# Optimization experiments

Measured on AMD Instinct MI355X. Metric: run time of the kernel, lower is better.

Reference implementation:

```python
import jax, jax.numpy as jnp
import numpy as np

PAD = 0
N_SENSE = 3
VOCAB = 100000
OUT_VOCAB = 50000
D = 128
B = 64
MAX_LEN = 512


def setup_inputs() -> dict:
    key = jax.random.key(0)
    ks = jax.random.split(key, 8)
    inputs = jax.random.randint(ks[0], (B, MAX_LEN * N_SENSE), 0, VOCAB, dtype=jnp.int64 if jax.config.jax_enable_x64 else jnp.int32)
    length_weights = jax.random.uniform(ks[1], (B, 1, 1), dtype=jnp.float32, minval=0.1, maxval=1.0)
    word_attn_mask = jax.random.bernoulli(ks[2], 0.1, (B, MAX_LEN))
    embedding = jax.random.normal(ks[3], (VOCAB, D), dtype=jnp.float32) * 0.02
    W_attn = jax.random.normal(ks[4], (1, D), dtype=jnp.float32) * 0.02
    b_attn = jnp.zeros((1,), dtype=jnp.float32)
    W_lin = jax.random.normal(ks[5], (OUT_VOCAB, D), dtype=jnp.float32) * 0.02
    b_lin = jnp.zeros((OUT_VOCAB,), dtype=jnp.float32)
    return {"inputs": inputs, "length_weights": length_weights, "word_attn_mask": word_attn_mask,
            "embedding": embedding, "W_attn": W_attn, "b_attn": b_attn, "W_lin": W_lin, "b_lin": b_lin}


def reference(inputs, length_weights, word_attn_mask, embedding, W_attn, b_attn, W_lin, b_lin):
    Bsz, LS = inputs.shape
    L = LS // N_SENSE
    # padding row contributes zeros (nn.Embedding padding_idx=PAD)
    E = embedding.at[PAD].set(0.0)
    embeds = E[inputs]                                   # [B, L*S, D]
    embeds4 = embeds.reshape(Bsz, L, N_SENSE, -1)
    embed_mean = embeds4.mean(axis=2)                    # [B, L, D]
    # word-level attention: Linear(D,1) -> mask -> softmax over words
    word_imp = jnp.einsum('bld,d->bl', embed_mean, W_attn[0]) + b_attn[0]
    word_imp = jnp.where(word_attn_mask, -jnp.inf, word_imp)
    word_w = jax.nn.softmax(word_imp, axis=-1)           # [B, L]
    context = jnp.einsum('bl,bld->bd', word_w, embed_mean)  # [B, D]
    # sense-level attention: similarity of each sense embedding to context
    sim = jnp.einsum('bnd,bd->bn', embeds, context)      # [B, L*S]
    sense_w = jax.nn.softmax(sim.reshape(Bsz, L, N_SENSE), axis=-1).reshape(Bsz, LS)
    attn_w = length_weights.reshape(Bsz, 1) * sense_w    # scale by 1/length
    attn_w = jnp.where(inputs == PAD, 0.0, attn_w)
    hidden = jnp.einsum('bn,bnd->bd', attn_w, embeds)    # [B, D]
    logits = hidden @ W_lin.T + b_lin                    # [B, OUT_VOCAB]
    return jax.nn.log_softmax(logits, axis=-1)
```

## Files before the change

### kernel.cpp

```cpp
#include <hip/hip_runtime.h>
#include <math.h>

#define B_    64
#define L_    512
#define S_    3
#define D_    128
#define OV_   50000
#define VOC_  100000
#define NBLK_ 782

typedef __attribute__((ext_vector_type(8))) short bf16x8;
typedef __attribute__((ext_vector_type(4))) float f32x4;

__device__ __forceinline__ float waveReduceSum(float v) {
#pragma unroll
    for (int off = 32; off >= 1; off >>= 1) v += __shfl_xor(v, off, 64);
    return v;
}
__device__ __forceinline__ float waveReduceMax(float v) {
#pragma unroll
    for (int off = 32; off >= 1; off >>= 1) v = fmaxf(v, __shfl_xor(v, off, 64));
    return v;
}

__device__ __forceinline__ short f2bf(float f) {
    unsigned int u = __float_as_uint(f);
    return (short)((u + 0x7FFFu + ((u >> 16) & 1u)) >> 16);
}

__global__ __launch_bounds__(256) void prequery_kernel(
    const float* __restrict__ emb, const float* __restrict__ Wa,
    float* __restrict__ P, float* __restrict__ context,
    float* __restrict__ hidden)
{
    const int tid = threadIdx.x;
    if (blockIdx.x < 64 && tid < D_) {
        context[blockIdx.x * D_ + tid] = 0.f;
        hidden[blockIdx.x * D_ + tid]  = 0.f;
    }

    const int lane = tid & 63;
    const int q = lane >> 4;
    const int j = lane & 15;
    const int waveg = blockIdx.x * 4 + (tid >> 6);
    const int nwaves = gridDim.x * 4;

    const float4 wa0 = ((const float4*)Wa)[2 * j];
    const float4 wa1 = ((const float4*)Wa)[2 * j + 1];

    for (int r0 = waveg * 4; r0 < VOC_; r0 += nwaves * 4) {
        const float4* row = (const float4*)(emb + (long)(r0 + q) * D_ + j * 8);
        float4 e0 = row[0], e1 = row[1];
        float s = e0.x * wa0.x + e0.y * wa0.y + e0.z * wa0.z + e0.w * wa0.w
                + e1.x * wa1.x + e1.y * wa1.y + e1.z * wa1.z + e1.w * wa1.w;
#pragma unroll
        for (int off = 8; off >= 1; off >>= 1) s += __shfl_xor(s, off, 64);
        if (j == 0) P[r0 + q] = s;
    }
}

__device__ __forceinline__ void word_softmax(
    const int* in_b, const int* __restrict__ mask, const float* __restrict__ P,
    float babias, int b, float* s_imp, float* s_red)
{
    const int tid = threadIdx.x;
    const int wave = tid >> 6, lane = tid & 63;

    int   idx[2][S_];
    float pv[2][S_];
#pragma unroll
    for (int half = 0; half < 2; ++half) {
        const int l = tid + half * 256;
#pragma unroll
        for (int s = 0; s < S_; ++s) {
            idx[half][s] = in_b[l * S_ + s];
            pv[half][s]  = P[idx[half][s]];
        }
    }
#pragma unroll
    for (int half = 0; half < 2; ++half) {
        const int l = tid + half * 256;
        float acc = 0.f;
#pragma unroll
        for (int s = 0; s < S_; ++s)
            acc += (idx[half][s] != 0) ? pv[half][s] : 0.f;
        float imp = acc * (1.0f / 3.0f) + babias;
        s_imp[l] = mask[b * L_ + l] ? -INFINITY : imp;
    }
    __syncthreads();

    float v0 = s_imp[tid], v1 = s_imp[tid + 256];
    float m = waveReduceMax(fmaxf(v0, v1));
    if (lane == 0) s_red[wave] = m;
    __syncthreads();
    m = fmaxf(fmaxf(s_red[0], s_red[1]), fmaxf(s_red[2], s_red[3]));
    __syncthreads();
    float p0 = expf(v0 - m), p1 = expf(v1 - m);
    float ssum = waveReduceSum(p0 + p1);
    if (lane == 0) s_red[wave] = ssum;
    __syncthreads();
    float inv = (1.0f / 3.0f) / (s_red[0] + s_red[1] + s_red[2] + s_red[3]);
    s_imp[tid]       = p0 * inv;
    s_imp[tid + 256] = p1 * inv;
    __syncthreads();
}

__global__ __launch_bounds__(256) void context_kernel(
    const int* __restrict__ inputs, const int* __restrict__ mask,
    const float* __restrict__ P, const float* __restrict__ ba,
    const float* __restrict__ emb, float* __restrict__ context)
{
    const int b    = blockIdx.x >> 4;
    const int base = (blockIdx.x & 15) * 32;
    const int tid  = threadIdx.x;
    const int wave = tid >> 6, lane = tid & 63;
    const int h = lane >> 5, j = lane & 31;

    __shared__ float s_imp[L_];
    __shared__ float s_red[4];
    __shared__ float s_part[8][D_];
    __shared__ int   s_idx[32 * S_];

    const int* in_b = inputs + b * (L_ * S_);
    if (tid < 32 * S_) s_idx[tid] = in_b[base * S_ + tid];
    word_softmax(in_b, mask, P, ba[0], b, s_imp, s_red);

    int    idx[4][S_];
    float4 e[4][S_];
#pragma unroll
    for (int it = 0; it < 4; ++it) {
        const int lw = (wave + it * 4) * 2 + h;
#pragma unroll
        for (int s = 0; s < S_; ++s) {
            idx[it][s] = s_idx[lw * S_ + s];
            e[it][s]   = ((const float4*)(emb + (long)idx[it][s] * D_))[j];
        }
    }

    float4 c = make_float4(0.f, 0.f, 0.f, 0.f);
#pragma unroll
    for (int it = 0; it < 4; ++it) {
        const int lw = (wave + it * 4) * 2 + h;
        const float w = s_imp[base + lw];
#pragma unroll
        for (int s = 0; s < S_; ++s) {
            const float ws = (idx[it][s] != 0) ? w : 0.f;
            c.x += ws * e[it][s].x; c.y += ws * e[it][s].y;
            c.z += ws * e[it][s].z; c.w += ws * e[it][s].w;
        }
    }
    ((float4*)s_part[wave * 2 + h])[j] = c;
    __syncthreads();
    if (tid < D_) {
        float acc = 0.f;
#pragma unroll
        for (int p = 0; p < 8; ++p) acc += s_part[p][tid];
        atomicAdd(&context[b * D_ + tid], acc);
    }
}

__global__ __launch_bounds__(256) void sense_kernel(
    const int* __restrict__ inputs, const float* __restrict__ lwp,
    const float* __restrict__ context, const float* __restrict__ emb,
    float* __restrict__ hidden)
{
    const int b    = blockIdx.x >> 5;
    const int base = (blockIdx.x & 31) * 16;
    const int tid  = threadIdx.x;
    const int wave = tid >> 6, lane = tid & 63;
    const int h = lane >> 5, j = lane & 31;

    __shared__ float s_part[8][D_];
    __shared__ int   s_idx[16 * S_];

    const int* in_b = inputs + b * (L_ * S_);
    if (tid < 16 * S_) s_idx[tid] = in_b[base * S_ + tid];
    __syncthreads();

    const float lwb = lwp[b];
    const float4 c4 = ((const float4*)(context + b * D_))[j];

    int    idx[2][S_];
    float4 e[2][S_];
#pragma unroll
    for (int it = 0; it < 2; ++it) {
        const int lw = (wave + it * 4) * 2 + h;
#pragma unroll
        for (int s = 0; s < S_; ++s) {
            idx[it][s] = s_idx[lw * S_ + s];
            e[it][s]   = ((const float4*)(emb + (long)idx[it][s] * D_))[j];
        }
    }

    float4 hacc = make_float4(0.f, 0.f, 0.f, 0.f);
#pragma unroll
    for (int it = 0; it < 2; ++it) {
        float sim[S_];
#pragma unroll
        for (int s = 0; s < S_; ++s)
            sim[s] = e[it][s].x * c4.x + e[it][s].y * c4.y
                   + e[it][s].z * c4.z + e[it][s].w * c4.w;
#pragma unroll
        for (int off = 16; off >= 1; off >>= 1) {
            sim[0] += __shfl_xor(sim[0], off, 64);
            sim[1] += __shfl_xor(sim[1], off, 64);
            sim[2] += __shfl_xor(sim[2], off, 64);
        }
        sim[0] = (idx[it][0] != 0) ? sim[0] : 0.f;
        sim[1] = (idx[it][1] != 0) ? sim[1] : 0.f;
        sim[2] = (idx[it][2] != 0) ? sim[2] : 0.f;
        float e0 = expf(sim[0]), e1 = expf(sim[1]), e2 = expf(sim[2]);
        float f = lwb / (e0 + e1 + e2);
        float w0 = (idx[it][0] != 0) ? e0 * f : 0.f;
        float w1 = (idx[it][1] != 0) ? e1 * f : 0.f;
        float w2 = (idx[it][2] != 0) ? e2 * f : 0.f;
        hacc.x += w0 * e[it][0].x + w1 * e[it][1].x + w2 * e[it][2].x;
        hacc.y += w0 * e[it][0].y + w1 * e[it][1].y + w2 * e[it][2].y;
        hacc.z += w0 * e[it][0].z + w1 * e[it][1].z + w2 * e[it][2].z;
        hacc.w += w0 * e[it][0].w + w1 * e[it][1].w + w2 * e[it][2].w;
    }
    ((float4*)s_part[wave * 2 + h])[j] = hacc;
    __syncthreads();
    if (tid < D_) {
        float acc = 0.f;
#pragma unroll
        for (int p = 0; p < 8; ++p) acc += s_part[p][tid];
        atomicAdd(&hidden[b * D_ + tid], acc);
    }
}

__global__ __launch_bounds__(256) void logits_kernel(
    const float* __restrict__ hidden, const float* __restrict__ Wl,
    const float* __restrict__ bl, float* __restrict__ logits,
    float* __restrict__ pS)
{
    __shared__ short s_hbf[64][136];
    const int tid  = threadIdx.x;
    const int wave = tid >> 6, lane = tid & 63;
    const int m15  = lane & 15, quad = lane >> 4;
    const int v    = blockIdx.x * 64 + wave * 16 + m15;
    const bool valid = (v < OV_);
    const int vc   = valid ? v : (OV_ - 1);

    for (int i = tid; i < 2048; i += 256) {
        float4 x = ((const float4*)hidden)[i];
        const int r = i >> 5;
        const int c = (i & 31) * 4;
        short* dst = &s_hbf[r][c];
        dst[0] = f2bf(x.x); dst[1] = f2bf(x.y);
        dst[2] = f2bf(x.z); dst[3] = f2bf(x.w);
    }
    __syncthreads();

    f32x4 acc[4];
#pragma unroll
    for (int t = 0; t < 4; ++t) acc[t] = (f32x4){0.f, 0.f, 0.f, 0.f};

    const float* wrow = Wl + (long)vc * D_ + quad * 8;
#pragma unroll
    for (int ks = 0; ks < 4; ++ks) {
        float4 x0 = *(const float4*)(wrow + ks * 32);
        float4 x1 = *(const float4*)(wrow + ks * 32 + 4);
        bf16x8 bfr;
        bfr[0] = f2bf(x0.x); bfr[1] = f2bf(x0.y); bfr[2] = f2bf(x0.z); bfr[3] = f2bf(x0.w);
        bfr[4] = f2bf(x1.x); bfr[5] = f2bf(x1.y); bfr[6] = f2bf(x1.z); bfr[7] = f2bf(x1.w);
#pragma unroll
        for (int t = 0; t < 4; ++t) {
            bf16x8 afr = *(const bf16x8*)&s_hbf[t * 16 + m15][ks * 32 + quad * 8];
            acc[t] = __builtin_amdgcn_mfma_f32_16x16x32_bf16(afr, bfr,
                                                             acc[t], 0, 0, 0);
        }
    }
    const float bias = bl[vc];
    if (valid) {
#pragma unroll
        for (int t = 0; t < 4; ++t)
#pragma unroll
            for (int r = 0; r < 4; ++r) {
                const int row = t * 16 + quad * 4 + r;
                logits[(long)row * OV_ + v] = acc[t][r] + bias;
            }
    }

    __shared__ float s_ps[64][4];
#pragma unroll
    for (int t = 0; t < 4; ++t) {
#pragma unroll
        for (int r = 0; r < 4; ++r) {
            float se = valid ? expf(acc[t][r] + bias) : 0.f;
#pragma unroll
            for (int off = 8; off >= 1; off >>= 1) se += __shfl_xor(se, off, 64);
            if (m15 == 0) s_ps[t * 16 + quad * 4 + r][wave] = se;
        }
    }
    __syncthreads();
    if (tid < 64)
        pS[tid * NBLK_ + blockIdx.x] = s_ps[tid][0] + s_ps[tid][1]
                                     + s_ps[tid][2] + s_ps[tid][3];
}

__global__ __launch_bounds__(256) void finalize_kernel(
    const float* __restrict__ logits, const float* __restrict__ pS,
    float* __restrict__ out)
{
    const int b     = blockIdx.x / 49;
    const int chunk = blockIdx.x % 49;
    const int tid   = threadIdx.x;
    const int wave  = tid >> 6, lane = tid & 63;

    __shared__ float s_red[4];
    __shared__ float s_logz;

    const float* rs = pS + b * NBLK_;
    float s = 0.f;
    for (int i = tid; i < NBLK_; i += 256) s += rs[i];
    s = waveReduceSum(s);
    if (lane == 0) s_red[wave] = s;
    __syncthreads();
    if (tid == 0) s_logz = logf(s_red[0] + s_red[1] + s_red[2] + s_red[3]);
    __syncthreads();
    const float z = s_logz;

    const int i4 = chunk * 256 + tid;
    if (i4 < OV_ / 4) {
        float4 x = ((const float4*)(logits + (long)b * OV_))[i4];
        x.x -= z; x.y -= z; x.z -= z; x.w -= z;
        ((float4*)(out + (long)b * OV_))[i4] = x;
    }
}

extern "C" void kernel_launch(void* const* d_in, const int* in_sizes, int n_in,
                              void* d_out, int out_size, void* d_ws, size_t ws_size,
                              hipStream_t stream) {
    const int*   inputs = (const int*)d_in[0];
    const float* lw     = (const float*)d_in[1];
    const int*   mask   = (const int*)d_in[2];
    const float* emb    = (const float*)d_in[3];
    const float* Wa     = (const float*)d_in[4];
    const float* ba     = (const float*)d_in[5];
    const float* Wl     = (const float*)d_in[6];
    const float* bl     = (const float*)d_in[7];
    float* out = (float*)d_out;

    float* ws = (float*)d_ws;
    float* hidden  = ws;
    float* context = ws + 8192;
    float* P       = ws + 16384;
    float* logits  = ws + 116384 + 96;
    float* pS      = logits + (long)B_ * OV_;

    prequery_kernel<<<625, 256, 0, stream>>>(emb, Wa, P, context, hidden);
    context_kernel<<<B_ * 16, 256, 0, stream>>>(inputs, mask, P, ba, emb, context);
    sense_kernel<<<B_ * 32, 256, 0, stream>>>(inputs, lw, context, emb, hidden);
    logits_kernel<<<NBLK_, 256, 0, stream>>>(hidden, Wl, bl, logits, pS);
    finalize_kernel<<<B_ * 49, 256, 0, stream>>>(logits, pS, out);
}
```

Baseline: 154.5 us.

## Split word softmax into its own kernel and halve context block work

Before, each of the 16 context blocks per batch recomputed the full 512-word softmax, gathering P for all 1536 tokens. That softmax now runs once per batch in a separate kernel that writes normalized word weights to workspace and also zeroes context and hidden. The context kernel then reads only its own 16 weights and handles 16 words per block over twice as many blocks. This removes redundant gathers and reductions at the cost of one extra kernel launch and a round trip through global memory.

```diff
diff --git a/kernel.cpp b/kernel.cpp
--- a/kernel.cpp
+++ b/kernel.cpp
@@ -30,15 +30,9 @@
 
 __global__ __launch_bounds__(256) void prequery_kernel(
     const float* __restrict__ emb, const float* __restrict__ Wa,
-    float* __restrict__ P, float* __restrict__ context,
-    float* __restrict__ hidden)
+    float* __restrict__ P)
 {
     const int tid = threadIdx.x;
-    if (blockIdx.x < 64 && tid < D_) {
-        context[blockIdx.x * D_ + tid] = 0.f;
-        hidden[blockIdx.x * D_ + tid]  = 0.f;
-    }
-
     const int lane = tid & 63;
     const int q = lane >> 4;
     const int j = lane & 15;
@@ -59,12 +53,23 @@
     }
 }
 
-__device__ __forceinline__ void word_softmax(
-    const int* in_b, const int* __restrict__ mask, const float* __restrict__ P,
-    float babias, int b, float* s_imp, float* s_red)
-{
+__global__ __launch_bounds__(256) void wordsoftmax_kernel(
+    const int* __restrict__ inputs, const int* __restrict__ mask,
+    const float* __restrict__ P, const float* __restrict__ ba,
+    float* __restrict__ wword, float* __restrict__ context,
+    float* __restrict__ hidden)
+{
+    const int b   = blockIdx.x;
     const int tid = threadIdx.x;
     const int wave = tid >> 6, lane = tid & 63;
+
+    if (tid < D_) { context[b * D_ + tid] = 0.f; hidden[b * D_ + tid] = 0.f; }
+
+    __shared__ float s_imp[L_];
+    __shared__ float s_red[4];
+
+    const int* in_b = inputs + b * (L_ * S_);
+    const float babias = ba[0];
 
     int   idx[2][S_];
     float pv[2][S_];
@@ -100,35 +105,33 @@
     if (lane == 0) s_red[wave] = ssum;
     __syncthreads();
     float inv = (1.0f / 3.0f) / (s_red[0] + s_red[1] + s_red[2] + s_red[3]);
-    s_imp[tid]       = p0 * inv;
-    s_imp[tid + 256] = p1 * inv;
-    __syncthreads();
+    wword[b * L_ + tid]       = p0 * inv;
+    wword[b * L_ + tid + 256] = p1 * inv;
 }
 
 __global__ __launch_bounds__(256) void context_kernel(
-    const int* __restrict__ inputs, const int* __restrict__ mask,
-    const float* __restrict__ P, const float* __restrict__ ba,
+    const int* __restrict__ inputs, const float* __restrict__ wword,
     const float* __restrict__ emb, float* __restrict__ context)
 {
-    const int b    = blockIdx.x >> 4;
-    const int base = (blockIdx.x & 15) * 32;
+    const int b    = blockIdx.x >> 5;
+    const int base = (blockIdx.x & 31) * 16;
     const int tid  = threadIdx.x;
     const int wave = tid >> 6, lane = tid & 63;
     const int h = lane >> 5, j = lane & 31;
 
-    __shared__ float s_imp[L_];
-    __shared__ float s_red[4];
     __shared__ float s_part[8][D_];
-    __shared__ int   s_idx[32 * S_];
+    __shared__ int   s_idx[16 * S_];
+    __shared__ float s_w[16];
 
     const int* in_b = inputs + b * (L_ * S_);
-    if (tid < 32 * S_) s_idx[tid] = in_b[base * S_ + tid];
-    word_softmax(in_b, mask, P, ba[0], b, s_imp, s_red);
-
-    int    idx[4][S_];
-    float4 e[4][S_];
-#pragma unroll
-    for (int it = 0; it < 4; ++it) {
+    if (tid < 16 * S_) s_idx[tid] = in_b[base * S_ + tid];
+    else if (tid >= 64 && tid < 80) s_w[tid - 64] = wword[b * L_ + base + tid - 64];
+    __syncthreads();
+
+    int    idx[2][S_];
+    float4 e[2][S_];
+#pragma unroll
+    for (int it = 0; it < 2; ++it) {
         const int lw = (wave + it * 4) * 2 + h;
 #pragma unroll
         for (int s = 0; s < S_; ++s) {
@@ -139,9 +142,9 @@
 
     float4 c = make_float4(0.f, 0.f, 0.f, 0.f);
 #pragma unroll
-    for (int it = 0; it < 4; ++it) {
+    for (int it = 0; it < 2; ++it) {
         const int lw = (wave + it * 4) * 2 + h;
-        const float w = s_imp[base + lw];
+        const float w = s_w[lw];
 #pragma unroll
         for (int s = 0; s < S_; ++s) {
             const float ws = (idx[it][s] != 0) ? w : 0.f;
@@ -346,11 +349,14 @@
     float* hidden  = ws;
     float* context = ws + 8192;
     float* P       = ws + 16384;
-    float* logits  = ws + 116384 + 96;
+    float* wword   = ws + 116384;
+    float* logits  = ws + 149152;
     float* pS      = logits + (long)B_ * OV_;
 
-    prequery_kernel<<<625, 256, 0, stream>>>(emb, Wa, P, context, hidden);
-    context_kernel<<<B_ * 16, 256, 0, stream>>>(inputs, mask, P, ba, emb, context);
+    prequery_kernel<<<625, 256, 0, stream>>>(emb, Wa, P);
+    wordsoftmax_kernel<<<B_, 256, 0, stream>>>(inputs, mask, P, ba, wword,
+                                               context, hidden);
+    context_kernel<<<B_ * 32, 256, 0, stream>>>(inputs, wword, emb, context);
     sense_kernel<<<B_ * 32, 256, 0, stream>>>(inputs, lw, context, emb, hidden);
     logits_kernel<<<NBLK_, 256, 0, stream>>>(hidden, Wl, bl, logits, pS);
     finalize_kernel<<<B_ * 49, 256, 0, stream>>>(logits, pS, out);
```

Measured after the change: 156.4 us. No clear change (+1.2%).
